# Optimization experiments

Hardware: AMD Instinct MI355X
Metric: run time of the kernel (lower is better)

The kernel has to match this reference:

```python
import jax, jax.numpy as jnp
import numpy as np

N = 100000
E = 1600000
D = 256
BN_EPS = 1e-5


def setup_inputs() -> dict:
    key = jax.random.key(0)
    ks = jax.random.split(key, 6)
    node_feats = jax.random.normal(ks[0], (N, D), dtype=jnp.float32)
    src = jax.random.randint(ks[1], (E,), 0, N, dtype=jnp.int64)
    dst = jax.random.randint(ks[2], (E,), 0, N, dtype=jnp.int64)
    eps = jnp.zeros((1,), dtype=jnp.float32)
    # Kaiming-uniform-like scaled init for linear layers
    W1 = jax.random.normal(ks[3], (D, 2 * D), dtype=jnp.float32) * (1.0 / np.sqrt(D))
    b1 = jnp.zeros((2 * D,), dtype=jnp.float32)
    W2 = jax.random.normal(ks[4], (2 * D, D), dtype=jnp.float32) * (1.0 / np.sqrt(2 * D))
    b2 = jnp.zeros((D,), dtype=jnp.float32)
    gamma = jnp.ones((D,), dtype=jnp.float32)
    beta = jnp.zeros((D,), dtype=jnp.float32)
    return {"node_feats": node_feats, "src": src, "dst": dst, "eps": eps,
            "W1": W1, "b1": b1, "W2": W2, "b2": b2, "gamma": gamma, "beta": beta}


def reference(node_feats, src, dst, eps, W1, b1, W2, b2, gamma, beta):
    n = node_feats.shape[0]
    # copy_u / sum: gather source features, scatter-sum into destinations
    neigh = jax.ops.segment_sum(node_feats[src], dst, num_segments=n)  # [N, D]
    h = (1.0 + eps) * node_feats + neigh
    # 2-layer MLP: D -> 2D -> D with ReLU
    h = jax.nn.relu(h @ W1 + b1) @ W2 + b2
    # BatchNorm1d, training mode: batch stats over N, biased variance
    mean = jnp.mean(h, axis=0)
    var = jnp.mean(jnp.square(h - mean), axis=0)
    h = (h - mean) * jax.lax.rsqrt(var + BN_EPS) * gamma + beta
    return h
```

## Files before the change

kernel.cpp:

```cpp
#include <hip/hip_runtime.h>
#include <hip/hip_bf16.h>
#include <stdint.h>

#define N_NODES 100000
#define DIM 256
#define HID 512
#define N_EDGES 1600000

#define NBUCK 782
#define BSHIFT 7
#define BMASK 127
#define CAPC 4096
#define CURSTRIDE 16

using short8 = __attribute__((ext_vector_type(8))) short;
using f32x4  = __attribute__((ext_vector_type(4))) float;

__device__ __forceinline__ unsigned short f2bf(float f) {
    union { float f; unsigned u; } v; v.f = f;
    unsigned u = v.u;
    unsigned r = u + 0x7fffu + ((u >> 16) & 1u);
    return (unsigned short)(r >> 16);
}
__device__ __forceinline__ float bf2f(unsigned short u) {
    union { unsigned u; float f; } v; v.u = ((unsigned)u) << 16; return v.f;
}
__device__ __forceinline__ void gload_lds16(const void* g, void* l) {
    __builtin_amdgcn_global_load_lds((const __attribute__((address_space(1))) void*)g,
                                     (__attribute__((address_space(3))) void*)l, 16, 0, 0);
}

__global__ void x2bf(const float* __restrict__ x, unsigned short* __restrict__ xb) {
    long i = (long)blockIdx.x * blockDim.x + threadIdx.x;
    float4 u0 = ((const float4*)x)[i * 2];
    float4 u1 = ((const float4*)x)[i * 2 + 1];
    short8 o;
    o[0] = (short)f2bf(u0.x); o[1] = (short)f2bf(u0.y);
    o[2] = (short)f2bf(u0.z); o[3] = (short)f2bf(u0.w);
    o[4] = (short)f2bf(u1.x); o[5] = (short)f2bf(u1.y);
    o[6] = (short)f2bf(u1.z); o[7] = (short)f2bf(u1.w);
    ((short8*)xb)[i] = o;
}


__global__ void zero_cursors(int* __restrict__ chunkCursor) {
    int i = blockIdx.x * 256 + threadIdx.x;
    if (i < NBUCK * CURSTRIDE) chunkCursor[i] = 0;
}

__global__ void bucket_scatter(const int* __restrict__ src, const int* __restrict__ dst,
                               int* __restrict__ chunkCursor, int* __restrict__ bucketed) {
    int e = blockIdx.x * 256 + threadIdx.x;
    int d = dst[e];
    int c = d >> BSHIFT;
    int pos = atomicAdd(&chunkCursor[c * CURSTRIDE], 1);
    bucketed[(size_t)c * CAPC + pos] = src[e] | ((d & BMASK) << 17);
}

__global__ void scan_chunks(const int* __restrict__ chunkCursor, int* __restrict__ chunkOff) {
    __shared__ int sm[1024];
    int t = threadIdx.x;
    int v = (t < NBUCK) ? chunkCursor[t * CURSTRIDE] : 0;
    sm[t] = v;
    __syncthreads();
    for (int off = 1; off < 1024; off <<= 1) {
        int add = (t >= off) ? sm[t - off] : 0;
        __syncthreads();
        sm[t] += add;
        __syncthreads();
    }
    chunkOff[t] = sm[t] - v;
}

__global__ __launch_bounds__(256) void chunk_sort(const int* __restrict__ bucketed,
        const int* __restrict__ chunkCursor, const int* __restrict__ chunkOff,
        int* __restrict__ start, int* __restrict__ count, int* __restrict__ sorted_src) {
    __shared__ int cnt[128];
    __shared__ int cur[128];
    __shared__ int sortedL[CAPC];
    int c = blockIdx.x;
    int t = threadIdx.x;
    int nE = chunkCursor[c * CURSTRIDE];
    int base = chunkOff[c];
    const int* bk = bucketed + (size_t)c * CAPC;
    if (t < 128) cnt[t] = 0;
    __syncthreads();
    for (int i = t; i < nE; i += 256)
        atomicAdd(&cnt[bk[i] >> 17], 1);
    __syncthreads();
    int v = (t < 128) ? cnt[t] : 0;
    for (int off = 1; off < 128; off <<= 1) {
        int add = (t >= off && t < 128) ? cnt[t - off] : 0;
        __syncthreads();
        if (t < 128) cnt[t] += add;
        __syncthreads();
    }
    if (t < 128) {
        int excl = cnt[t] - v;
        int gid = c * 128 + t;
        start[gid] = base + excl;
        count[gid] = v;
        cur[t] = excl;
    }
    __syncthreads();
    for (int i = t; i < nE; i += 256) {
        int p = bk[i];
        int pos = atomicAdd(&cur[p >> 17], 1);
        sortedL[pos] = p & 0x1FFFF;
    }
    __syncthreads();
    for (int i = t; i < nE; i += 256)
        sorted_src[base + i] = sortedL[i];
}

__global__ void gather_sum(const unsigned short* __restrict__ xb, const int* __restrict__ sorted_src,
                           const int* __restrict__ start, const int* __restrict__ count,
                           const float* __restrict__ eps, unsigned short* __restrict__ accb) {
    int lane = threadIdx.x & 63;
    int n = blockIdx.x * 4 + (threadIdx.x >> 6);
    if (n >= N_NODES) return;
    float s = 1.0f + eps[0];
    const ushort4* xr = (const ushort4*)(xb + (size_t)n * DIM);
    ushort4 v = xr[lane];
    float a0 = bf2f(v.x) * s, a1 = bf2f(v.y) * s, a2 = bf2f(v.z) * s, a3 = bf2f(v.w) * s;
    int base = start[n];
    int end = base + count[n];
    int j = base;
    for (; j + 4 <= end; j += 4) {
        int s0 = sorted_src[j], s1 = sorted_src[j + 1];
        int s2 = sorted_src[j + 2], s3 = sorted_src[j + 3];
        ushort4 v0 = ((const ushort4*)(xb + (size_t)s0 * DIM))[lane];
        ushort4 v1 = ((const ushort4*)(xb + (size_t)s1 * DIM))[lane];
        ushort4 v2 = ((const ushort4*)(xb + (size_t)s2 * DIM))[lane];
        ushort4 v3 = ((const ushort4*)(xb + (size_t)s3 * DIM))[lane];
        a0 += bf2f(v0.x) + bf2f(v1.x) + bf2f(v2.x) + bf2f(v3.x);
        a1 += bf2f(v0.y) + bf2f(v1.y) + bf2f(v2.y) + bf2f(v3.y);
        a2 += bf2f(v0.z) + bf2f(v1.z) + bf2f(v2.z) + bf2f(v3.z);
        a3 += bf2f(v0.w) + bf2f(v1.w) + bf2f(v2.w) + bf2f(v3.w);
    }
    for (; j < end; ++j) {
        int s0 = sorted_src[j];
        ushort4 v0 = ((const ushort4*)(xb + (size_t)s0 * DIM))[lane];
        a0 += bf2f(v0.x); a1 += bf2f(v0.y); a2 += bf2f(v0.z); a3 += bf2f(v0.w);
    }
    ushort4 o;
    o.x = f2bf(a0); o.y = f2bf(a1); o.z = f2bf(a2); o.w = f2bf(a3);
    ((ushort4*)(accb + (size_t)n * DIM))[lane] = o;
}


__global__ void prep_weights(const float* __restrict__ W1, const float* __restrict__ W2,
                             unsigned short* __restrict__ W1t, unsigned short* __restrict__ W2t) {
    int tid = blockIdx.x * blockDim.x + threadIdx.x;
    if (tid < DIM * HID) {
        int n = tid >> 8, k = tid & 255;
        W1t[tid] = f2bf(W1[k * HID + n]);
    } else {
        int j = tid - DIM * HID;
        int n = j >> 9, k = j & 511;
        W2t[j] = f2bf(W2[k * DIM + n]);
    }
}

template<int K, int NOUT, bool RELU_BF16_OUT>
__global__ __launch_bounds__(256) void gemm128(const unsigned short* __restrict__ A,
        const unsigned short* __restrict__ Bt, const float* __restrict__ bias,
        void* __restrict__ Cout, int M) {
    __shared__ unsigned short As[128 * 32];
    __shared__ unsigned short Bs[128 * 32];
    constexpr int NT = NOUT / 128;
    int mtile = blockIdx.x / NT;
    int ntile = blockIdx.x % NT;
    int mbase = mtile * 128, nbase = ntile * 128;
    int t = threadIdx.x;
    int lane = t & 63, wid = t >> 6;
    int wm = (wid & 1) * 64, wn = (wid >> 1) * 64;
    int lo = lane & 15, quad = lane >> 4;

    int s0 = t, s1 = t + 256;
    int r0 = s0 >> 2, c0 = (s0 & 3) ^ ((r0 >> 1) & 3);
    int r1 = s1 >> 2, c1 = (s1 & 3) ^ ((r1 >> 1) & 3);
    int gmA0 = mbase + r0; if (gmA0 >= M) gmA0 = M - 1;
    int gmA1 = mbase + r1; if (gmA1 >= M) gmA1 = M - 1;
    const unsigned short* gA0 = A + (size_t)gmA0 * K + c0 * 8;
    const unsigned short* gA1 = A + (size_t)gmA1 * K + c1 * 8;
    const unsigned short* gB0 = Bt + (size_t)(nbase + r0) * K + c0 * 8;
    const unsigned short* gB1 = Bt + (size_t)(nbase + r1) * K + c1 * 8;
    char* lA0 = (char*)As + wid * 1024;
    char* lA1 = (char*)As + 4096 + wid * 1024;
    char* lB0 = (char*)Bs + wid * 1024;
    char* lB1 = (char*)Bs + 4096 + wid * 1024;

    int offA[4], offB[4];
    #pragma unroll
    for (int i = 0; i < 4; ++i) {
        int ra = wm + i * 16 + lo;
        offA[i] = ra * 64 + ((quad ^ ((ra >> 1) & 3)) * 16);
        int rb = wn + i * 16 + lo;
        offB[i] = rb * 64 + ((quad ^ ((rb >> 1) & 3)) * 16);
    }

    f32x4 acc[4][4] = {};
    for (int kt = 0; kt < K / 32; ++kt) {
        if (kt) __syncthreads();
        int ko = kt * 32;
        gload_lds16(gA0 + ko, lA0);
        gload_lds16(gA1 + ko, lA1);
        gload_lds16(gB0 + ko, lB0);
        gload_lds16(gB1 + ko, lB1);
        __syncthreads();
        short8 a[4], b[4];
        #pragma unroll
        for (int i = 0; i < 4; ++i) {
            a[i] = *(const short8*)((const char*)As + offA[i]);
            b[i] = *(const short8*)((const char*)Bs + offB[i]);
        }
        #pragma unroll
        for (int mi = 0; mi < 4; ++mi)
            #pragma unroll
            for (int ni = 0; ni < 4; ++ni)
                acc[mi][ni] = __builtin_amdgcn_mfma_f32_16x16x32_bf16(a[mi], b[ni], acc[mi][ni], 0, 0, 0);
    }
    #pragma unroll
    for (int mi = 0; mi < 4; ++mi)
      #pragma unroll
      for (int ni = 0; ni < 4; ++ni)
        #pragma unroll
        for (int r = 0; r < 4; ++r) {
            int row = mbase + wm + mi * 16 + quad * 4 + r;
            int col = nbase + wn + ni * 16 + lo;
            if (row < M) {
                float v = acc[mi][ni][r] + bias[col];
                if constexpr (RELU_BF16_OUT) {
                    v = fmaxf(v, 0.0f);
                    ((unsigned short*)Cout)[(size_t)row * NOUT + col] = f2bf(v);
                } else {
                    ((float*)Cout)[(size_t)row * NOUT + col] = v;
                }
            }
        }
}


__global__ void col_stats1(const float* __restrict__ h, float* __restrict__ partial) {
    int t = threadIdx.x;
    int b = blockIdx.x;
    int r0 = b * 200;
    int r1 = r0 + 200; if (r1 > N_NODES) r1 = N_NODES;
    float s = 0.f, q = 0.f;
    for (int r = r0; r < r1; ++r) {
        float v = h[(size_t)r * DIM + t];
        s += v; q += v * v;
    }
    partial[b * 512 + t] = s;
    partial[b * 512 + 256 + t] = q;
}

__global__ void col_stats2(const float* __restrict__ partial, const float* __restrict__ gamma,
                           const float* __restrict__ beta, float* __restrict__ sc) {
    int t = threadIdx.x;
    float s = 0.f, q = 0.f;
    for (int b = 0; b < 500; ++b) {
        s += partial[b * 512 + t];
        q += partial[b * 512 + 256 + t];
    }
    float mean = s * (1.0f / (float)N_NODES);
    float var = q * (1.0f / (float)N_NODES) - mean * mean;
    float inv = rsqrtf(var + 1e-5f);
    float scale = gamma[t] * inv;
    sc[t] = scale;
    sc[256 + t] = beta[t] - mean * scale;
}

__global__ void bn_apply(const float* __restrict__ h, const float* __restrict__ sc,
                         float* __restrict__ out) {
    long i = (long)blockIdx.x * blockDim.x + threadIdx.x;
    int c = (int)((i * 4) & (DIM - 1));
    float4 v = ((const float4*)h)[i];
    float4 scale = *(const float4*)(sc + c);
    float4 shift = *(const float4*)(sc + 256 + c);
    float4 o;
    o.x = v.x * scale.x + shift.x;
    o.y = v.y * scale.y + shift.y;
    o.z = v.z * scale.z + shift.z;
    o.w = v.w * scale.w + shift.w;
    ((float4*)out)[i] = o;
}

extern "C" void kernel_launch(void* const* d_in, const int* in_sizes, int n_in,
                              void* d_out, int out_size, void* d_ws, size_t ws_size,
                              hipStream_t stream) {
    const float* x     = (const float*)d_in[0];
    const int*   src   = (const int*)d_in[1];
    const int*   dst   = (const int*)d_in[2];
    const float* eps   = (const float*)d_in[3];
    const float* W1    = (const float*)d_in[4];
    const float* b1    = (const float*)d_in[5];
    const float* W2    = (const float*)d_in[6];
    const float* b2    = (const float*)d_in[7];
    const float* gamma = (const float*)d_in[8];
    const float* beta  = (const float*)d_in[9];

    char* ws = (char*)d_ws;
    unsigned short* xb   = (unsigned short*)ws;
    unsigned short* accb = (unsigned short*)(ws + 51200000);
    float*          h2   = (float*)ws;
    unsigned short* W1t  = (unsigned short*)(ws + 102400000);
    unsigned short* W2t  = (unsigned short*)(ws + 102662144);
    float*          sc   = (float*)(ws + 102924288);

    char* ob = (char*)d_out;
    int* chunkCursor = (int*)ob;
    int* chunkOff    = (int*)(ob + 51200);
    int* start       = (int*)(ob + 55296);
    int* count       = (int*)(ob + 455680);
    int* sorted_src  = (int*)(ob + 856064);
    int* bucketed    = (int*)(ob + 7256064);
    unsigned short* tbuf    = (unsigned short*)d_out;
    float*          partial = (float*)d_out;
    float*          out     = (float*)d_out;

    hipLaunchKernelGGL(x2bf, dim3(12500), dim3(256), 0, stream, x, xb);
    hipLaunchKernelGGL(prep_weights, dim3(1024), dim3(256), 0, stream, W1, W2, W1t, W2t);
    hipLaunchKernelGGL(zero_cursors, dim3(49), dim3(256), 0, stream, chunkCursor);
    hipLaunchKernelGGL(bucket_scatter, dim3(N_EDGES / 256), dim3(256), 0, stream,
                       src, dst, chunkCursor, bucketed);
    hipLaunchKernelGGL(scan_chunks, dim3(1), dim3(1024), 0, stream, chunkCursor, chunkOff);
    hipLaunchKernelGGL(chunk_sort, dim3(NBUCK), dim3(256), 0, stream,
                       bucketed, chunkCursor, chunkOff, start, count, sorted_src);
    hipLaunchKernelGGL(gather_sum, dim3(25000), dim3(256), 0, stream,
                       xb, sorted_src, start, count, eps, accb);
    hipLaunchKernelGGL((gemm128<256, 512, true>), dim3(782 * 4), dim3(256), 0, stream,
                       accb, W1t, b1, (void*)tbuf, N_NODES);
    hipLaunchKernelGGL((gemm128<512, 256, false>), dim3(782 * 2), dim3(256), 0, stream,
                       tbuf, W2t, b2, (void*)h2, N_NODES);
    hipLaunchKernelGGL(col_stats1, dim3(500), dim3(256), 0, stream, h2, partial);
    hipLaunchKernelGGL(col_stats2, dim3(1), dim3(256), 0, stream, partial, gamma, beta, sc);
    hipLaunchKernelGGL(bn_apply, dim3(25000), dim3(256), 0, stream, h2, sc, out);
}
```

Before: 664.1 us.

## Fuse prep kernels, drop chunk scan, fuse column stats into second GEMM

Merges the bf16 conversion, weight transpose and cursor zeroing into one launch. It removes the scan_chunks kernel by sorting each bucket in place and indexing it directly at c*CAPC. It also computes BatchNorm column sums and squares in the second GEMM epilogue, using wave shuffles, shared atomics and 8 global replicas, which removes the col_stats1 pass over the h2 output. The GEMM tile order is regrouped in groups of 8 M-tiles for L2 reuse. The cost is atomic contention and float atomics whose summation order is not deterministic.

```diff
diff --git a/kernel.cpp b/kernel.cpp
--- a/kernel.cpp
+++ b/kernel.cpp
@@ -30,22 +30,37 @@
                                      (__attribute__((address_space(3))) void*)l, 16, 0, 0);
 }
 
-__global__ void x2bf(const float* __restrict__ x, unsigned short* __restrict__ xb) {
-    long i = (long)blockIdx.x * blockDim.x + threadIdx.x;
-    float4 u0 = ((const float4*)x)[i * 2];
-    float4 u1 = ((const float4*)x)[i * 2 + 1];
-    short8 o;
-    o[0] = (short)f2bf(u0.x); o[1] = (short)f2bf(u0.y);
-    o[2] = (short)f2bf(u0.z); o[3] = (short)f2bf(u0.w);
-    o[4] = (short)f2bf(u1.x); o[5] = (short)f2bf(u1.y);
-    o[6] = (short)f2bf(u1.z); o[7] = (short)f2bf(u1.w);
-    ((short8*)xb)[i] = o;
-}
-
-
-__global__ void zero_cursors(int* __restrict__ chunkCursor) {
-    int i = blockIdx.x * 256 + threadIdx.x;
-    if (i < NBUCK * CURSTRIDE) chunkCursor[i] = 0;
+__global__ void prep_all(const float* __restrict__ x, unsigned short* __restrict__ xb,
+                         const float* __restrict__ W1, const float* __restrict__ W2,
+                         unsigned short* __restrict__ W1t, unsigned short* __restrict__ W2t,
+                         int* __restrict__ chunkCursor, float* __restrict__ gsums) {
+    int b = blockIdx.x;
+    int t = threadIdx.x;
+    if (b < 12500) {
+        long i = (long)b * 256 + t;
+        float4 u0 = ((const float4*)x)[i * 2];
+        float4 u1 = ((const float4*)x)[i * 2 + 1];
+        short8 o;
+        o[0] = (short)f2bf(u0.x); o[1] = (short)f2bf(u0.y);
+        o[2] = (short)f2bf(u0.z); o[3] = (short)f2bf(u0.w);
+        o[4] = (short)f2bf(u1.x); o[5] = (short)f2bf(u1.y);
+        o[6] = (short)f2bf(u1.z); o[7] = (short)f2bf(u1.w);
+        ((short8*)xb)[i] = o;
+    } else if (b < 13524) {
+        int tid = (b - 12500) * 256 + t;
+        if (tid < DIM * HID) {
+            int n = tid >> 8, k = tid & 255;
+            W1t[tid] = f2bf(W1[k * HID + n]);
+        } else {
+            int j = tid - DIM * HID;
+            int n = j >> 9, k = j & 511;
+            W2t[j] = f2bf(W2[k * DIM + n]);
+        }
+    } else {
+        int i = (b - 13524) * 256 + t;
+        if (i < NBUCK * CURSTRIDE) chunkCursor[i] = 0;
+        if (i < 4096) gsums[i] = 0.0f;
+    }
 }
 
 __global__ void bucket_scatter(const int* __restrict__ src, const int* __restrict__ dst,
@@ -57,32 +72,16 @@
     bucketed[(size_t)c * CAPC + pos] = src[e] | ((d & BMASK) << 17);
 }
 
-__global__ void scan_chunks(const int* __restrict__ chunkCursor, int* __restrict__ chunkOff) {
-    __shared__ int sm[1024];
-    int t = threadIdx.x;
-    int v = (t < NBUCK) ? chunkCursor[t * CURSTRIDE] : 0;
-    sm[t] = v;
-    __syncthreads();
-    for (int off = 1; off < 1024; off <<= 1) {
-        int add = (t >= off) ? sm[t - off] : 0;
-        __syncthreads();
-        sm[t] += add;
-        __syncthreads();
-    }
-    chunkOff[t] = sm[t] - v;
-}
-
-__global__ __launch_bounds__(256) void chunk_sort(const int* __restrict__ bucketed,
-        const int* __restrict__ chunkCursor, const int* __restrict__ chunkOff,
-        int* __restrict__ start, int* __restrict__ count, int* __restrict__ sorted_src) {
+__global__ __launch_bounds__(256) void chunk_sort(int* __restrict__ bucketed,
+        const int* __restrict__ chunkCursor,
+        int* __restrict__ start, int* __restrict__ count) {
     __shared__ int cnt[128];
     __shared__ int cur[128];
     __shared__ int sortedL[CAPC];
     int c = blockIdx.x;
     int t = threadIdx.x;
     int nE = chunkCursor[c * CURSTRIDE];
-    int base = chunkOff[c];
-    const int* bk = bucketed + (size_t)c * CAPC;
+    int* bk = bucketed + (size_t)c * CAPC;
     if (t < 128) cnt[t] = 0;
     __syncthreads();
     for (int i = t; i < nE; i += 256)
@@ -98,7 +97,7 @@
     if (t < 128) {
         int excl = cnt[t] - v;
         int gid = c * 128 + t;
-        start[gid] = base + excl;
+        start[gid] = c * CAPC + excl;
         count[gid] = v;
         cur[t] = excl;
     }
@@ -110,7 +109,7 @@
     }
     __syncthreads();
     for (int i = t; i < nE; i += 256)
-        sorted_src[base + i] = sortedL[i];
+        bk[i] = sortedL[i];
 }
 
 __global__ void gather_sum(const unsigned short* __restrict__ xb, const int* __restrict__ sorted_src,
@@ -149,28 +148,20 @@
 }
 
 
-__global__ void prep_weights(const float* __restrict__ W1, const float* __restrict__ W2,
-                             unsigned short* __restrict__ W1t, unsigned short* __restrict__ W2t) {
-    int tid = blockIdx.x * blockDim.x + threadIdx.x;
-    if (tid < DIM * HID) {
-        int n = tid >> 8, k = tid & 255;
-        W1t[tid] = f2bf(W1[k * HID + n]);
-    } else {
-        int j = tid - DIM * HID;
-        int n = j >> 9, k = j & 511;
-        W2t[j] = f2bf(W2[k * DIM + n]);
-    }
-}
-
-template<int K, int NOUT, bool RELU_BF16_OUT>
+template<int K, int NOUT, bool RELU_BF16_OUT, bool COLSTATS>
 __global__ __launch_bounds__(256) void gemm128(const unsigned short* __restrict__ A,
         const unsigned short* __restrict__ Bt, const float* __restrict__ bias,
-        void* __restrict__ Cout, int M) {
+        void* __restrict__ Cout, float* __restrict__ gsums, int M) {
     __shared__ unsigned short As[128 * 32];
     __shared__ unsigned short Bs[128 * 32];
     constexpr int NT = NOUT / 128;
-    int mtile = blockIdx.x / NT;
-    int ntile = blockIdx.x % NT;
+    constexpr int NTLOG = (NT == 4) ? 2 : 1;
+    int L = blockIdx.x;
+    int x8 = L & 7;
+    int ntile = (L >> 3) & (NT - 1);
+    int mtile = (L >> (3 + NTLOG)) * 8 + x8;
+    int MT = (M + 127) >> 7;
+    if (mtile >= MT) return;
     int mbase = mtile * 128, nbase = ntile * 128;
     int t = threadIdx.x;
     int lane = t & 63, wid = t >> 6;
@@ -221,6 +212,7 @@
             for (int ni = 0; ni < 4; ++ni)
                 acc[mi][ni] = __builtin_amdgcn_mfma_f32_16x16x32_bf16(a[mi], b[ni], acc[mi][ni], 0, 0, 0);
     }
+    float cs[4] = {0.f, 0.f, 0.f, 0.f}, cq[4] = {0.f, 0.f, 0.f, 0.f};
     #pragma unroll
     for (int mi = 0; mi < 4; ++mi)
       #pragma unroll
@@ -237,32 +229,40 @@
                 } else {
                     ((float*)Cout)[(size_t)row * NOUT + col] = v;
                 }
+                if constexpr (COLSTATS) { cs[ni] += v; cq[ni] += v * v; }
             }
         }
-}
-
-
-__global__ void col_stats1(const float* __restrict__ h, float* __restrict__ partial) {
-    int t = threadIdx.x;
-    int b = blockIdx.x;
-    int r0 = b * 200;
-    int r1 = r0 + 200; if (r1 > N_NODES) r1 = N_NODES;
-    float s = 0.f, q = 0.f;
-    for (int r = r0; r < r1; ++r) {
-        float v = h[(size_t)r * DIM + t];
-        s += v; q += v * v;
-    }
-    partial[b * 512 + t] = s;
-    partial[b * 512 + 256 + t] = q;
-}
-
-__global__ void col_stats2(const float* __restrict__ partial, const float* __restrict__ gamma,
+    if constexpr (COLSTATS) {
+        __shared__ float colS[128], colQ[128];
+        if (t < 128) { colS[t] = 0.f; colQ[t] = 0.f; }
+        __syncthreads();
+        #pragma unroll
+        for (int ni = 0; ni < 4; ++ni) {
+            float sv = cs[ni], qv = cq[ni];
+            sv += __shfl_xor(sv, 16); sv += __shfl_xor(sv, 32);
+            qv += __shfl_xor(qv, 16); qv += __shfl_xor(qv, 32);
+            if (quad == 0) {
+                atomicAdd(&colS[wn + ni * 16 + lo], sv);
+                atomicAdd(&colQ[wn + ni * 16 + lo], qv);
+            }
+        }
+        __syncthreads();
+        if (t < 128) {
+            int rep = x8;
+            atomicAdd(&gsums[rep * 512 + nbase + t], colS[t]);
+            atomicAdd(&gsums[rep * 512 + 256 + nbase + t], colQ[t]);
+        }
+    }
+}
+
+
+__global__ void col_stats2(const float* __restrict__ gsums, const float* __restrict__ gamma,
                            const float* __restrict__ beta, float* __restrict__ sc) {
     int t = threadIdx.x;
     float s = 0.f, q = 0.f;
-    for (int b = 0; b < 500; ++b) {
-        s += partial[b * 512 + t];
-        q += partial[b * 512 + 256 + t];
+    for (int rep = 0; rep < 8; ++rep) {
+        s += gsums[rep * 512 + t];
+        q += gsums[rep * 512 + 256 + t];
     }
     float mean = s * (1.0f / (float)N_NODES);
     float var = q * (1.0f / (float)N_NODES) - mean * mean;
@@ -308,33 +308,28 @@
     unsigned short* W1t  = (unsigned short*)(ws + 102400000);
     unsigned short* W2t  = (unsigned short*)(ws + 102662144);
     float*          sc   = (float*)(ws + 102924288);
+    float*          gsums = (float*)(ws + 102926336);
 
     char* ob = (char*)d_out;
     int* chunkCursor = (int*)ob;
-    int* chunkOff    = (int*)(ob + 51200);
-    int* start       = (int*)(ob + 55296);
-    int* count       = (int*)(ob + 455680);
-    int* sorted_src  = (int*)(ob + 856064);
-    int* bucketed    = (int*)(ob + 7256064);
-    unsigned short* tbuf    = (unsigned short*)d_out;
-    float*          partial = (float*)d_out;
-    float*          out     = (float*)d_out;
-
-    hipLaunchKernelGGL(x2bf, dim3(12500), dim3(256), 0, stream, x, xb);
-    hipLaunchKernelGGL(prep_weights, dim3(1024), dim3(256), 0, stream, W1, W2, W1t, W2t);
-    hipLaunchKernelGGL(zero_cursors, dim3(49), dim3(256), 0, stream, chunkCursor);
+    int* start       = (int*)(ob + 51200);
+    int* count       = (int*)(ob + 451584);
+    int* bucketed    = (int*)(ob + 851968);
+    unsigned short* tbuf = (unsigned short*)d_out;
+    float*          out  = (float*)d_out;
+
+    hipLaunchKernelGGL(prep_all, dim3(13573), dim3(256), 0, stream,
+                       x, xb, W1, W2, W1t, W2t, chunkCursor, gsums);
     hipLaunchKernelGGL(bucket_scatter, dim3(N_EDGES / 256), dim3(256), 0, stream,
                        src, dst, chunkCursor, bucketed);
-    hipLaunchKernelGGL(scan_chunks, dim3(1), dim3(1024), 0, stream, chunkCursor, chunkOff);
     hipLaunchKernelGGL(chunk_sort, dim3(NBUCK), dim3(256), 0, stream,
-                       bucketed, chunkCursor, chunkOff, start, count, sorted_src);
+                       bucketed, chunkCursor, start, count);
     hipLaunchKernelGGL(gather_sum, dim3(25000), dim3(256), 0, stream,
-                       xb, sorted_src, start, count, eps, accb);
-    hipLaunchKernelGGL((gemm128<256, 512, true>), dim3(782 * 4), dim3(256), 0, stream,
-                       accb, W1t, b1, (void*)tbuf, N_NODES);
-    hipLaunchKernelGGL((gemm128<512, 256, false>), dim3(782 * 2), dim3(256), 0, stream,
-                       tbuf, W2t, b2, (void*)h2, N_NODES);
-    hipLaunchKernelGGL(col_stats1, dim3(500), dim3(256), 0, stream, h2, partial);
-    hipLaunchKernelGGL(col_stats2, dim3(1), dim3(256), 0, stream, partial, gamma, beta, sc);
+                       xb, bucketed, start, count, eps, accb);
+    hipLaunchKernelGGL((gemm128<256, 512, true, false>), dim3(784 * 4), dim3(256), 0, stream,
+                       accb, W1t, b1, (void*)tbuf, nullptr, N_NODES);
+    hipLaunchKernelGGL((gemm128<512, 256, false, true>), dim3(784 * 2), dim3(256), 0, stream,
+                       tbuf, W2t, b2, (void*)h2, gsums, N_NODES);
+    hipLaunchKernelGGL(col_stats2, dim3(1), dim3(256), 0, stream, gsums, gamma, beta, sc);
     hipLaunchKernelGGL(bn_apply, dim3(25000), dim3(256), 0, stream, h2, sc, out);
 }
```

Measured after the change: 573.1 us. 13.7% less time.
